# Kernel optimization log

Measured on AMD Instinct MI355X. Metric: run time of the kernel, lower is better.

## Reference

```python
import jax, jax.numpy as jnp
import numpy as np

HID = 4096
NH = 64
HD = HID // NH            # 64
ROT = int(0.5 * HD)       # 32, partial rotary
THETA = 25000.0
EPS = 1e-5
NEG = jnp.finfo(jnp.float32).min


def setup_inputs() -> dict:
    key = jax.random.key(0)
    ks = jax.random.split(key, 8)
    B, S = 1, 2048
    hidden_states = jax.random.normal(ks[0], (B, S, HID), dtype=jnp.float32)
    # causal additive mask [B,1,S,S]
    causal = jnp.where(jnp.tril(jnp.ones((S, S), dtype=bool)), 0.0, NEG)
    attention_mask = jnp.broadcast_to(causal, (B, 1, S, S)).astype(jnp.float32)
    position_ids = jnp.broadcast_to(jnp.arange(S, dtype=jnp.int32), (B, S))
    sc = 1.0 / np.sqrt(HID)
    W_qkv = jax.random.normal(ks[1], (HID, 3 * HID), dtype=jnp.float32) * sc
    b_qkv = jnp.zeros((3 * HID,), dtype=jnp.float32)
    W_dense = jax.random.normal(ks[2], (HID, HID), dtype=jnp.float32) * sc
    b_dense = jnp.zeros((HID,), dtype=jnp.float32)
    q_ln_w = jnp.ones((HD,), dtype=jnp.float32)
    q_ln_b = jnp.zeros((HD,), dtype=jnp.float32)
    k_ln_w = jnp.ones((HD,), dtype=jnp.float32)
    k_ln_b = jnp.zeros((HD,), dtype=jnp.float32)
    return dict(hidden_states=hidden_states, attention_mask=attention_mask,
                position_ids=position_ids, W_qkv=W_qkv, b_qkv=b_qkv,
                W_dense=W_dense, b_dense=b_dense,
                q_ln_w=q_ln_w, q_ln_b=q_ln_b, k_ln_w=k_ln_w, k_ln_b=k_ln_b)


def _layernorm(x, w, b):
    mu = jnp.mean(x, axis=-1, keepdims=True)
    var = jnp.mean(jnp.square(x - mu), axis=-1, keepdims=True)
    return (x - mu) * jax.lax.rsqrt(var + EPS) * w + b


def _rope_cos_sin(seq_len, position_ids):
    inv_freq = 1.0 / (THETA ** (jnp.arange(0, ROT, 2, dtype=jnp.float32) / ROT))
    t = jnp.arange(seq_len, dtype=jnp.float32)
    freqs = jnp.einsum('s,f->sf', t, inv_freq)        # [S, ROT/2]
    emb = jnp.concatenate([freqs, freqs], axis=-1)    # [S, ROT]
    cos = jnp.cos(emb)[position_ids][:, None, :, :]   # [B,1,S,ROT]
    sin = jnp.sin(emb)[position_ids][:, None, :, :]
    return cos, sin


def _rotate_half(x):
    x1, x2 = jnp.split(x, 2, axis=-1)
    return jnp.concatenate([-x2, x1], axis=-1)


def reference(hidden_states, attention_mask, position_ids, W_qkv, b_qkv,
              W_dense, b_dense, q_ln_w, q_ln_b, k_ln_w, k_ln_b):
    B, S, _ = hidden_states.shape
    fused = hidden_states @ W_qkv + b_qkv                 # [B,S,3*HID]
    fused = fused.reshape(B, S, NH, 3, HD)
    q, k, v = fused[..., 0, :], fused[..., 1, :], fused[..., 2, :]  # [B,S,NH,HD]
    q = _layernorm(q, q_ln_w, q_ln_b)
    k = _layernorm(k, k_ln_w, k_ln_b)
    q = q.transpose(0, 2, 1, 3)                           # [B,NH,S,HD]
    k = k.transpose(0, 2, 1, 3)
    v = v.transpose(0, 2, 1, 3)
    cos, sin = _rope_cos_sin(S, position_ids)
    q_rot, q_pass = q[..., :ROT], q[..., ROT:]
    k_rot, k_pass = k[..., :ROT], k[..., ROT:]
    q_rot = q_rot * cos + _rotate_half(q_rot) * sin
    k_rot = k_rot * cos + _rotate_half(k_rot) * sin
    q = jnp.concatenate([q_rot, q_pass], axis=-1)
    k = jnp.concatenate([k_rot, k_pass], axis=-1)
    scores = jnp.einsum('bhqd,bhkd->bhqk', q, k) / np.sqrt(HD)
    scores = scores + attention_mask
    probs = jax.nn.softmax(scores.astype(jnp.float32), axis=-1).astype(q.dtype)
    attn = jnp.einsum('bhqk,bhkd->bhqd', probs, v)        # [B,NH,S,HD]
    attn = attn.transpose(0, 2, 1, 3).reshape(B, S, HID)
    return attn @ W_dense + b_dense
```

## Files before the change

kernel.cpp:

```cpp
#include <hip/hip_runtime.h>
#include <hip/hip_bf16.h>


typedef __attribute__((ext_vector_type(4))) unsigned int u32x4;
typedef __attribute__((ext_vector_type(8))) __bf16 bf16x8;
typedef __attribute__((ext_vector_type(4))) float f32x4;

__device__ __forceinline__ bf16x8 frag_ld(const __hip_bfloat16* p) {
  return __builtin_bit_cast(bf16x8, *(const u32x4*)p);
}

__device__ __forceinline__ void gll16(const __hip_bfloat16* g,
                                      __hip_bfloat16* l) {
  __builtin_amdgcn_global_load_lds(
      (const __attribute__((address_space(1))) unsigned int*)g,
      (__attribute__((address_space(3))) unsigned int*)l, 16, 0, 0);
}

__global__ __launch_bounds__(256) void cvt_kernel(
    const float* __restrict__ in, __hip_bfloat16* __restrict__ out, int n4) {
  int i = blockIdx.x * 256 + threadIdx.x;
  if (i < n4) {
    float4 v = ((const float4*)in)[i];
    union { __hip_bfloat16 h[4]; unsigned long long u; } pk;
    pk.h[0] = __float2bfloat16(v.x);
    pk.h[1] = __float2bfloat16(v.y);
    pk.h[2] = __float2bfloat16(v.z);
    pk.h[3] = __float2bfloat16(v.w);
    ((unsigned long long*)out)[i] = pk.u;
  }
}

__global__ __launch_bounds__(256) void transpose_kernel(
    const float* __restrict__ W, __hip_bfloat16* __restrict__ WT,
    int K, int ldW, int colStride, int colOff) {
  __shared__ __align__(16) __hip_bfloat16 tile[64 * 72];
  const int t = threadIdx.x;
  const int c0 = blockIdx.x * colStride + colOff;
  const int n0 = blockIdx.x * 64;
  const int k0 = blockIdx.y * 64;
  for (int c = t; c < 1024; c += 256) {
    int row = c >> 4, col4 = (c & 15) << 2;
    float4 v = *(const float4*)&W[(size_t)(k0 + row) * ldW + c0 + col4];
    union { __hip_bfloat16 h[4]; unsigned long long u; } pk;
    pk.h[0] = __float2bfloat16(v.x);
    pk.h[1] = __float2bfloat16(v.y);
    pk.h[2] = __float2bfloat16(v.z);
    pk.h[3] = __float2bfloat16(v.w);
    *(unsigned long long*)&tile[row * 72 + col4] = pk.u;
  }
  __syncthreads();
  for (int c = t; c < 512; c += 256) {
    int row = c >> 3, col8 = (c & 7) << 3;
    union { __hip_bfloat16 h[8]; u32x4 v; } pk;
#pragma unroll
    for (int j = 0; j < 8; ++j) pk.h[j] = tile[(col8 + j) * 72 + row];
    *(u32x4*)&WT[(size_t)(n0 + row) * K + k0 + col8] = pk.v;
  }
}

__global__ __launch_bounds__(512, 2) void gemm256_kernel(
    const __hip_bfloat16* __restrict__ A, const __hip_bfloat16* __restrict__ BT,
    const float* __restrict__ bias, float* __restrict__ Cf,
    __hip_bfloat16* __restrict__ Cb, const float* __restrict__ lnw,
    const float* __restrict__ lnb, const int* __restrict__ pos,
    int M, int N, int K, int mode) {
  __shared__ __align__(16) __hip_bfloat16 As[3][128 * 64];
  __shared__ __align__(16) __hip_bfloat16 Bs[3][256 * 64];
  const int t = threadIdx.x;
  const int wv = t >> 6, lane = t & 63;
  const int qd = lane >> 4, md = lane & 15;
  const int wr = wv >> 2, wc = wv & 3;
  const int bid = blockIdx.x;
  const int swz = (bid & 7) * 32 + (bid >> 3);
  const int m0 = (swz >> 4) * 128, n0 = (swz & 15) * 256;
  const int rA = t >> 3;
  const int cg = (t & 7) ^ (rA & 7);
  const __hip_bfloat16* pA0 = A + (size_t)(m0 + rA) * K + cg * 8;
  const __hip_bfloat16* pA1 = A + (size_t)(m0 + 64 + rA) * K + cg * 8;
  const __hip_bfloat16* pB0 = BT + (size_t)(n0 + rA) * K + cg * 8;
  const __hip_bfloat16* pB1 = BT + (size_t)(n0 + 64 + rA) * K + cg * 8;
  const __hip_bfloat16* pB2 = BT + (size_t)(n0 + 128 + rA) * K + cg * 8;
  const __hip_bfloat16* pB3 = BT + (size_t)(n0 + 192 + rA) * K + cg * 8;
  const int ldsW = wv * 8 * 64;
  const int aRow = (wr * 64 + md) * 64;
  const int bRow = (wc * 64 + md) * 64;
  const int sw0 = (qd ^ (md & 7)) << 3;
  const int sw1 = ((4 + qd) ^ (md & 7)) << 3;
  f32x4 acc[4][4] = {};

  gll16(pA0, &As[0][ldsW]);
  gll16(pA1, &As[0][64 * 64 + ldsW]);
  gll16(pB0, &Bs[0][ldsW]);
  gll16(pB1, &Bs[0][64 * 64 + ldsW]);
  gll16(pB2, &Bs[0][128 * 64 + ldsW]);
  gll16(pB3, &Bs[0][192 * 64 + ldsW]);
  gll16(pA0 + 64, &As[1][ldsW]);
  gll16(pA1 + 64, &As[1][64 * 64 + ldsW]);
  gll16(pB0 + 64, &Bs[1][ldsW]);
  gll16(pB1 + 64, &Bs[1][64 * 64 + ldsW]);
  gll16(pB2 + 64, &Bs[1][128 * 64 + ldsW]);
  gll16(pB3 + 64, &Bs[1][192 * 64 + ldsW]);
  asm volatile("s_waitcnt vmcnt(6)" ::: "memory");
  __builtin_amdgcn_s_barrier();

  int cur = 0, nb = 2;
  for (int kt = 0; kt < 64; ++kt) {
    const __hip_bfloat16* Ac = As[cur];
    const __hip_bfloat16* Bc = Bs[cur];
    const bool st = kt < 62;
    const int koff = (kt + 2) * 64;
    bf16x8 af[4], bf[4];
#pragma unroll
    for (int i = 0; i < 4; ++i) af[i] = frag_ld(&Ac[aRow + i * 1024 + sw0]);
#pragma unroll
    for (int i = 0; i < 4; ++i) bf[i] = frag_ld(&Bc[bRow + i * 1024 + sw0]);
    if (st) {
      gll16(pA0 + koff, &As[nb][ldsW]);
      gll16(pA1 + koff, &As[nb][64 * 64 + ldsW]);
      gll16(pB0 + koff, &Bs[nb][ldsW]);
    }
    __builtin_amdgcn_s_barrier();
    asm volatile("s_waitcnt lgkmcnt(0)" ::: "memory");
    __builtin_amdgcn_s_setprio(1);
#pragma unroll
    for (int mi = 0; mi < 4; ++mi)
#pragma unroll
      for (int ni = 0; ni < 4; ++ni)
        acc[mi][ni] = __builtin_amdgcn_mfma_f32_16x16x32_bf16(
            af[mi], bf[ni], acc[mi][ni], 0, 0, 0);
    __builtin_amdgcn_s_setprio(0);
    __builtin_amdgcn_s_barrier();
#pragma unroll
    for (int i = 0; i < 4; ++i) af[i] = frag_ld(&Ac[aRow + i * 1024 + sw1]);
#pragma unroll
    for (int i = 0; i < 4; ++i) bf[i] = frag_ld(&Bc[bRow + i * 1024 + sw1]);
    if (st) {
      gll16(pB1 + koff, &Bs[nb][64 * 64 + ldsW]);
      gll16(pB2 + koff, &Bs[nb][128 * 64 + ldsW]);
      gll16(pB3 + koff, &Bs[nb][192 * 64 + ldsW]);
    }
    __builtin_amdgcn_s_barrier();
    asm volatile("s_waitcnt lgkmcnt(0)" ::: "memory");
    __builtin_amdgcn_s_setprio(1);
#pragma unroll
    for (int mi = 0; mi < 4; ++mi)
#pragma unroll
      for (int ni = 0; ni < 4; ++ni)
        acc[mi][ni] = __builtin_amdgcn_mfma_f32_16x16x32_bf16(
            af[mi], bf[ni], acc[mi][ni], 0, 0, 0);
    __builtin_amdgcn_s_setprio(0);
    if (kt < 62)
      asm volatile("s_waitcnt vmcnt(6)" ::: "memory");
    else if (kt < 63)
      asm volatile("s_waitcnt vmcnt(0)" ::: "memory");
    __builtin_amdgcn_s_barrier();
    cur = (cur == 2) ? 0 : cur + 1;
    nb = (nb == 2) ? 0 : nb + 1;
  }
  if (mode == 0) {
#pragma unroll
    for (int ni = 0; ni < 4; ++ni) {
      int col = n0 + wc * 64 + ni * 16 + md;
      float bv = bias[col];
#pragma unroll
      for (int mi = 0; mi < 4; ++mi) {
        int rb = m0 + wr * 64 + mi * 16 + qd * 4;
#pragma unroll
        for (int r = 0; r < 4; ++r)
          Cf[(size_t)(rb + r) * N + col] = acc[mi][ni][r] + bv;
      }
    }
  } else {
    float g[4], bb[4], bv[4];
    int hd[4];
#pragma unroll
    for (int ni = 0; ni < 4; ++ni) {
      int col = n0 + wc * 64 + ni * 16 + md;
      hd[ni] = col;
      bv[ni] = bias[(col >> 6) * 192 + (col & 63)];
      if (mode >= 2) { g[ni] = lnw[ni * 16 + md]; bb[ni] = lnb[ni * 16 + md]; }
    }
    const float invf =
        (mode >= 2) ? powf(25000.0f, -(float)md / 16.0f) : 0.0f;
#pragma unroll
    for (int mi = 0; mi < 4; ++mi) {
#pragma unroll
      for (int r = 0; r < 4; ++r) {
        int row = m0 + wr * 64 + mi * 16 + qd * 4 + r;
        float v[4];
#pragma unroll
        for (int ni = 0; ni < 4; ++ni) v[ni] = acc[mi][ni][r] + bv[ni];
        if (mode >= 2) {
          float s = v[0] + v[1] + v[2] + v[3];
#pragma unroll
          for (int x = 1; x < 16; x <<= 1) s += __shfl_xor(s, x, 16);
          float mu = s * (1.0f / 64.0f);
          float ss = 0.0f;
#pragma unroll
          for (int ni = 0; ni < 4; ++ni) {
            v[ni] -= mu;
            ss += v[ni] * v[ni];
          }
#pragma unroll
          for (int x = 1; x < 16; x <<= 1) ss += __shfl_xor(ss, x, 16);
          float rs = rsqrtf(ss * (1.0f / 64.0f) + 1e-5f);
#pragma unroll
          for (int ni = 0; ni < 4; ++ni) v[ni] = v[ni] * rs * g[ni] + bb[ni];
          float sn, cs;
          sincosf((float)pos[row] * invf, &sn, &cs);
          float v0 = v[0], v1 = v[1];
          v[0] = v0 * cs - v1 * sn;
          v[1] = v1 * cs + v0 * sn;
          if (mode == 2) {
#pragma unroll
            for (int ni = 0; ni < 4; ++ni) v[ni] *= 0.18033688f;
          }
        }
#pragma unroll
        for (int ni = 0; ni < 4; ++ni)
          Cb[((size_t)(hd[ni] >> 6) * M + row) * 64 + (hd[ni] & 63)] =
              __float2bfloat16(v[ni]);
      }
    }
  }
}

__global__ __launch_bounds__(256) void vtrans_kernel(
    const __hip_bfloat16* __restrict__ V, __hip_bfloat16* __restrict__ VT) {
  const int h = blockIdx.x, s0 = blockIdx.y * 64, t = threadIdx.x;
  __shared__ __align__(16) __hip_bfloat16 vt[64 * 72];
  for (int c = t; c < 512; c += 256) {
    int r = c >> 3, col8 = (c & 7) << 3;
    *(u32x4*)&vt[r * 72 + col8] =
        *(const u32x4*)&V[((size_t)h * 2048 + s0 + r) * 64 + col8];
  }
  __syncthreads();
  for (int c = t; c < 512; c += 256) {
    int d = c >> 3, col8 = (c & 7) << 3;
    union { __hip_bfloat16 hh[8]; u32x4 v; } pk;
#pragma unroll
    for (int j = 0; j < 8; ++j) pk.hh[j] = vt[(col8 + j) * 72 + d];
    *(u32x4*)&VT[((size_t)h * 64 + d) * 2048 + s0 + col8] = pk.v;
  }
}

__global__ __launch_bounds__(256) void fattn_kernel(
    const __hip_bfloat16* __restrict__ Q, const __hip_bfloat16* __restrict__ K,
    const __hip_bfloat16* __restrict__ VT, __hip_bfloat16* __restrict__ attn) {
  const int h = blockIdx.x, qb = 31 - blockIdx.y;
  const int t = threadIdx.x, wv = t >> 6, lane = t & 63;
  const int qd = lane >> 4, md = lane & 15;
  __shared__ __align__(16) __hip_bfloat16 Kls[64 * 72];
  __shared__ __align__(16) __hip_bfloat16 Vls[64 * 72];
  __shared__ __align__(16) __hip_bfloat16 Pls[64 * 72];
  const int q0 = qb * 64;
  const __hip_bfloat16* Qp = Q + ((size_t)h * 2048 + q0 + wv * 16 + md) * 64;
  bf16x8 qf0 = frag_ld(Qp + qd * 8);
  bf16x8 qf1 = frag_ld(Qp + 32 + qd * 8);
  float lp[4] = {0.f, 0.f, 0.f, 0.f};
  f32x4 O[4] = {};
  for (int kb = 0; kb <= qb; ++kb) {
    __syncthreads();
    for (int c = t; c < 512; c += 256) {
      int row = c >> 3, col8 = (c & 7) << 3;
      *(u32x4*)&Kls[row * 72 + col8] =
          *(const u32x4*)&K[((size_t)h * 2048 + kb * 64 + row) * 64 + col8];
      *(u32x4*)&Vls[row * 72 + col8] =
          *(const u32x4*)&VT[((size_t)h * 64 + row) * 2048 + kb * 64 + col8];
    }
    __syncthreads();
    const bool diag = (kb == qb);
    float pv[4][4];
#pragma unroll
    for (int nt = 0; nt < 4; ++nt) {
      f32x4 s4 = {};
      bf16x8 kf0 = frag_ld(&Kls[(nt * 16 + md) * 72 + qd * 8]);
      bf16x8 kf1 = frag_ld(&Kls[(nt * 16 + md) * 72 + 32 + qd * 8]);
      s4 = __builtin_amdgcn_mfma_f32_16x16x32_bf16(qf0, kf0, s4, 0, 0, 0);
      s4 = __builtin_amdgcn_mfma_f32_16x16x32_bf16(qf1, kf1, s4, 0, 0, 0);
      int key = nt * 16 + md;
#pragma unroll
      for (int r = 0; r < 4; ++r) {
        float p = exp2f(s4[r]);
        if (diag) p = (key > wv * 16 + qd * 4 + r) ? 0.f : p;
        pv[nt][r] = p;
        lp[r] += p;
      }
    }
#pragma unroll
    for (int nt = 0; nt < 4; ++nt)
#pragma unroll
      for (int r = 0; r < 4; ++r)
        Pls[(wv * 16 + qd * 4 + r) * 72 + nt * 16 + md] =
            __float2bfloat16(pv[nt][r]);
    bf16x8 pf0 = frag_ld(&Pls[(wv * 16 + md) * 72 + qd * 8]);
    bf16x8 pf1 = frag_ld(&Pls[(wv * 16 + md) * 72 + 32 + qd * 8]);
#pragma unroll
    for (int nt = 0; nt < 4; ++nt) {
      bf16x8 vf0 = frag_ld(&Vls[(nt * 16 + md) * 72 + qd * 8]);
      bf16x8 vf1 = frag_ld(&Vls[(nt * 16 + md) * 72 + 32 + qd * 8]);
      O[nt] = __builtin_amdgcn_mfma_f32_16x16x32_bf16(pf0, vf0, O[nt], 0, 0, 0);
      O[nt] = __builtin_amdgcn_mfma_f32_16x16x32_bf16(pf1, vf1, O[nt], 0, 0, 0);
    }
  }
#pragma unroll
  for (int r = 0; r < 4; ++r) {
#pragma unroll
    for (int x = 1; x < 16; x <<= 1) lp[r] += __shfl_xor(lp[r], x, 16);
    lp[r] = 1.0f / lp[r];
  }
#pragma unroll
  for (int nt = 0; nt < 4; ++nt) {
    int col = h * 64 + nt * 16 + md;
#pragma unroll
    for (int r = 0; r < 4; ++r) {
      int row = q0 + wv * 16 + qd * 4 + r;
      attn[(size_t)row * 4096 + col] = __float2bfloat16(O[nt][r] * lp[r]);
    }
  }
}

extern "C" void kernel_launch(void* const* d_in, const int* in_sizes, int n_in,
                              void* d_out, int out_size, void* d_ws,
                              size_t ws_size, hipStream_t stream) {
  const float* hidden = (const float*)d_in[0];
  const int* pos = (const int*)d_in[2];
  const float* Wqkv = (const float*)d_in[3];
  const float* bqkv = (const float*)d_in[4];
  const float* Wd = (const float*)d_in[5];
  const float* bd = (const float*)d_in[6];
  const float* qlw = (const float*)d_in[7];
  const float* qlb = (const float*)d_in[8];
  const float* klw = (const float*)d_in[9];
  const float* klb = (const float*)d_in[10];

  char* ws = (char*)d_ws;
  __hip_bfloat16* WpT = (__hip_bfloat16*)ws;
  __hip_bfloat16* VT = (__hip_bfloat16*)ws;
  __hip_bfloat16* attn = (__hip_bfloat16*)(ws + 16777216);
  __hip_bfloat16* Hb = (__hip_bfloat16*)(ws + 33554432);
  __hip_bfloat16* Qb = (__hip_bfloat16*)(ws + 50331648);
  __hip_bfloat16* Kb = (__hip_bfloat16*)(ws + 67108864);
  __hip_bfloat16* Vb = (__hip_bfloat16*)(ws + 83886080);
  __hip_bfloat16* WdT = (__hip_bfloat16*)(ws + 33554432);
  float* out = (float*)d_out;

  cvt_kernel<<<8192, 256, 0, stream>>>(hidden, Hb, 2097152);
  __hip_bfloat16* qkv_dst[3] = {Qb, Kb, Vb};
  const float* lnw_p[3] = {qlw, klw, nullptr};
  const float* lnb_p[3] = {qlb, klb, nullptr};
  const int mode_p[3] = {2, 3, 1};
  for (int p = 0; p < 3; ++p) {
    transpose_kernel<<<dim3(64, 64), 256, 0, stream>>>(Wqkv, WpT, 4096, 12288,
                                                       192, p * 64);
    gemm256_kernel<<<256, 512, 0, stream>>>(Hb, WpT, bqkv + p * 64, nullptr,
                                            qkv_dst[p], lnw_p[p], lnb_p[p], pos,
                                            2048, 4096, 4096, mode_p[p]);
  }
  vtrans_kernel<<<dim3(64, 32), 256, 0, stream>>>(Vb, VT);
  fattn_kernel<<<dim3(64, 32), 256, 0, stream>>>(Qb, Kb, VT, attn);
  transpose_kernel<<<dim3(64, 64), 256, 0, stream>>>(Wd, WdT, 4096, 4096, 64, 0);
  gemm256_kernel<<<256, 512, 0, stream>>>(attn, WdT, bd, out, nullptr, nullptr,
                                          nullptr, nullptr, 2048, 4096, 4096,
                                          0);
}
```

Baseline: 762.6 us.

## Use 16-wave 1024-thread GEMM blocks with smaller per-wave tiles

Reworks the GEMM kernel to launch 1024 threads per block instead of 512. The 128x256 block tile stays the same, but each wave now computes 32x64 instead of 64x64, so it holds half the accumulators and issues fewer global-to-LDS loads per stage. The aim is more waves per CU for latency hiding within the same LDS triple buffer. In exchange, each wave does less MFMA work per LDS fragment load and per barrier, so barrier and LDS-read overhead rise relative to compute.

```diff
diff --git a/kernel.cpp b/kernel.cpp
--- a/kernel.cpp
+++ b/kernel.cpp
@@ -59,7 +59,7 @@
   }
 }
 
-__global__ __launch_bounds__(512, 2) void gemm256_kernel(
+__global__ __launch_bounds__(1024, 1) void gemm256_kernel(
     const __hip_bfloat16* __restrict__ A, const __hip_bfloat16* __restrict__ BT,
     const float* __restrict__ bias, float* __restrict__ Cf,
     __hip_bfloat16* __restrict__ Cb, const float* __restrict__ lnw,
@@ -72,36 +72,29 @@
   const int qd = lane >> 4, md = lane & 15;
   const int wr = wv >> 2, wc = wv & 3;
   const int bid = blockIdx.x;
-  const int swz = (bid & 7) * 32 + (bid >> 3);
-  const int m0 = (swz >> 4) * 128, n0 = (swz & 15) * 256;
+  const int cpx = gridDim.x >> 3;
+  const int swz = (bid & 7) * cpx + (bid >> 3);
+  const int nblk = N >> 8;
+  const int m0 = (swz / nblk) * 128, n0 = (swz % nblk) * 256;
   const int rA = t >> 3;
   const int cg = (t & 7) ^ (rA & 7);
-  const __hip_bfloat16* pA0 = A + (size_t)(m0 + rA) * K + cg * 8;
-  const __hip_bfloat16* pA1 = A + (size_t)(m0 + 64 + rA) * K + cg * 8;
+  const __hip_bfloat16* pA = A + (size_t)(m0 + rA) * K + cg * 8;
   const __hip_bfloat16* pB0 = BT + (size_t)(n0 + rA) * K + cg * 8;
-  const __hip_bfloat16* pB1 = BT + (size_t)(n0 + 64 + rA) * K + cg * 8;
-  const __hip_bfloat16* pB2 = BT + (size_t)(n0 + 128 + rA) * K + cg * 8;
-  const __hip_bfloat16* pB3 = BT + (size_t)(n0 + 192 + rA) * K + cg * 8;
-  const int ldsW = wv * 8 * 64;
-  const int aRow = (wr * 64 + md) * 64;
+  const __hip_bfloat16* pB1 = pB0 + (size_t)128 * K;
+  const int ldsW = wv * 512;
+  const int aRow = (wr * 32 + md) * 64;
   const int bRow = (wc * 64 + md) * 64;
   const int sw0 = (qd ^ (md & 7)) << 3;
   const int sw1 = ((4 + qd) ^ (md & 7)) << 3;
-  f32x4 acc[4][4] = {};
-
-  gll16(pA0, &As[0][ldsW]);
-  gll16(pA1, &As[0][64 * 64 + ldsW]);
+  f32x4 acc[2][4] = {};
+
+  gll16(pA, &As[0][ldsW]);
   gll16(pB0, &Bs[0][ldsW]);
-  gll16(pB1, &Bs[0][64 * 64 + ldsW]);
-  gll16(pB2, &Bs[0][128 * 64 + ldsW]);
-  gll16(pB3, &Bs[0][192 * 64 + ldsW]);
-  gll16(pA0 + 64, &As[1][ldsW]);
-  gll16(pA1 + 64, &As[1][64 * 64 + ldsW]);
+  gll16(pB1, &Bs[0][8192 + ldsW]);
+  gll16(pA + 64, &As[1][ldsW]);
   gll16(pB0 + 64, &Bs[1][ldsW]);
-  gll16(pB1 + 64, &Bs[1][64 * 64 + ldsW]);
-  gll16(pB2 + 64, &Bs[1][128 * 64 + ldsW]);
-  gll16(pB3 + 64, &Bs[1][192 * 64 + ldsW]);
-  asm volatile("s_waitcnt vmcnt(6)" ::: "memory");
+  gll16(pB1 + 64, &Bs[1][8192 + ldsW]);
+  asm volatile("s_waitcnt vmcnt(3)" ::: "memory");
   __builtin_amdgcn_s_barrier();
 
   int cur = 0, nb = 2;
@@ -110,21 +103,20 @@
     const __hip_bfloat16* Bc = Bs[cur];
     const bool st = kt < 62;
     const int koff = (kt + 2) * 64;
-    bf16x8 af[4], bf[4];
-#pragma unroll
-    for (int i = 0; i < 4; ++i) af[i] = frag_ld(&Ac[aRow + i * 1024 + sw0]);
+    bf16x8 af[2], bf[4];
+#pragma unroll
+    for (int i = 0; i < 2; ++i) af[i] = frag_ld(&Ac[aRow + i * 1024 + sw0]);
 #pragma unroll
     for (int i = 0; i < 4; ++i) bf[i] = frag_ld(&Bc[bRow + i * 1024 + sw0]);
     if (st) {
-      gll16(pA0 + koff, &As[nb][ldsW]);
-      gll16(pA1 + koff, &As[nb][64 * 64 + ldsW]);
+      gll16(pA + koff, &As[nb][ldsW]);
       gll16(pB0 + koff, &Bs[nb][ldsW]);
     }
     __builtin_amdgcn_s_barrier();
     asm volatile("s_waitcnt lgkmcnt(0)" ::: "memory");
     __builtin_amdgcn_s_setprio(1);
 #pragma unroll
-    for (int mi = 0; mi < 4; ++mi)
+    for (int mi = 0; mi < 2; ++mi)
 #pragma unroll
       for (int ni = 0; ni < 4; ++ni)
         acc[mi][ni] = __builtin_amdgcn_mfma_f32_16x16x32_bf16(
@@ -132,26 +124,24 @@
     __builtin_amdgcn_s_setprio(0);
     __builtin_amdgcn_s_barrier();
 #pragma unroll
-    for (int i = 0; i < 4; ++i) af[i] = frag_ld(&Ac[aRow + i * 1024 + sw1]);
+    for (int i = 0; i < 2; ++i) af[i] = frag_ld(&Ac[aRow + i * 1024 + sw1]);
 #pragma unroll
     for (int i = 0; i < 4; ++i) bf[i] = frag_ld(&Bc[bRow + i * 1024 + sw1]);
     if (st) {
-      gll16(pB1 + koff, &Bs[nb][64 * 64 + ldsW]);
-      gll16(pB2 + koff, &Bs[nb][128 * 64 + ldsW]);
-      gll16(pB3 + koff, &Bs[nb][192 * 64 + ldsW]);
+      gll16(pB1 + koff, &Bs[nb][8192 + ldsW]);
     }
     __builtin_amdgcn_s_barrier();
     asm volatile("s_waitcnt lgkmcnt(0)" ::: "memory");
     __builtin_amdgcn_s_setprio(1);
 #pragma unroll
-    for (int mi = 0; mi < 4; ++mi)
+    for (int mi = 0; mi < 2; ++mi)
 #pragma unroll
       for (int ni = 0; ni < 4; ++ni)
         acc[mi][ni] = __builtin_amdgcn_mfma_f32_16x16x32_bf16(
             af[mi], bf[ni], acc[mi][ni], 0, 0, 0);
     __builtin_amdgcn_s_setprio(0);
     if (kt < 62)
-      asm volatile("s_waitcnt vmcnt(6)" ::: "memory");
+      asm volatile("s_waitcnt vmcnt(3)" ::: "memory");
     else if (kt < 63)
       asm volatile("s_waitcnt vmcnt(0)" ::: "memory");
     __builtin_amdgcn_s_barrier();
@@ -164,8 +154,8 @@
       int col = n0 + wc * 64 + ni * 16 + md;
       float bv = bias[col];
 #pragma unroll
-      for (int mi = 0; mi < 4; ++mi) {
-        int rb = m0 + wr * 64 + mi * 16 + qd * 4;
+      for (int mi = 0; mi < 2; ++mi) {
+        int rb = m0 + wr * 32 + mi * 16 + qd * 4;
 #pragma unroll
         for (int r = 0; r < 4; ++r)
           Cf[(size_t)(rb + r) * N + col] = acc[mi][ni][r] + bv;
@@ -184,10 +174,10 @@
     const float invf =
         (mode >= 2) ? powf(25000.0f, -(float)md / 16.0f) : 0.0f;
 #pragma unroll
-    for (int mi = 0; mi < 4; ++mi) {
+    for (int mi = 0; mi < 2; ++mi) {
 #pragma unroll
       for (int r = 0; r < 4; ++r) {
-        int row = m0 + wr * 64 + mi * 16 + qd * 4 + r;
+        int row = m0 + wr * 32 + mi * 16 + qd * 4 + r;
         float v[4];
 #pragma unroll
         for (int ni = 0; ni < 4; ++ni) v[ni] = acc[mi][ni][r] + bv[ni];
@@ -354,14 +344,14 @@
   for (int p = 0; p < 3; ++p) {
     transpose_kernel<<<dim3(64, 64), 256, 0, stream>>>(Wqkv, WpT, 4096, 12288,
                                                        192, p * 64);
-    gemm256_kernel<<<256, 512, 0, stream>>>(Hb, WpT, bqkv + p * 64, nullptr,
-                                            qkv_dst[p], lnw_p[p], lnb_p[p], pos,
-                                            2048, 4096, 4096, mode_p[p]);
+    gemm256_kernel<<<256, 1024, 0, stream>>>(Hb, WpT, bqkv + p * 64, nullptr,
+                                             qkv_dst[p], lnw_p[p], lnb_p[p],
+                                             pos, 2048, 4096, 4096, mode_p[p]);
   }
   vtrans_kernel<<<dim3(64, 32), 256, 0, stream>>>(Vb, VT);
   fattn_kernel<<<dim3(64, 32), 256, 0, stream>>>(Qb, Kb, VT, attn);
   transpose_kernel<<<dim3(64, 64), 256, 0, stream>>>(Wd, WdT, 4096, 4096, 64, 0);
-  gemm256_kernel<<<256, 512, 0, stream>>>(attn, WdT, bd, out, nullptr, nullptr,
-                                          nullptr, nullptr, 2048, 4096, 4096,
-                                          0);
-}
+  gemm256_kernel<<<256, 1024, 0, stream>>>(attn, WdT, bd, out, nullptr, nullptr,
+                                           nullptr, nullptr, 2048, 4096, 4096,
+                                           0);
+}
```

Result: no change. 771.4 us (+1.2%).

## Double query tile per attention block to share K/V tile loads across 8 waves

Applied to the files above, without the earlier changes.

The flash-attention kernel now covers 128 query rows per block with 512 threads (two 64-row groups of four waves) and launches half as many blocks. Each K/V tile staged in LDS is reused by twice as many queries, which roughly halves global K/V traffic and shared-memory staging per query. Each wave gets its own P scratch buffer. The upper query group idles on the last key tile but still hits the barriers, and larger blocks mean fewer blocks in flight and a coarser causal load balance.

```diff
diff --git a/kernel.cpp b/kernel.cpp
--- a/kernel.cpp
+++ b/kernel.cpp
@@ -245,32 +245,35 @@
   }
 }
 
-__global__ __launch_bounds__(256) void fattn_kernel(
+__global__ __launch_bounds__(512) void fattn_kernel(
     const __hip_bfloat16* __restrict__ Q, const __hip_bfloat16* __restrict__ K,
     const __hip_bfloat16* __restrict__ VT, __hip_bfloat16* __restrict__ attn) {
-  const int h = blockIdx.x, qb = 31 - blockIdx.y;
+  const int h = blockIdx.x, qb = 15 - blockIdx.y;
   const int t = threadIdx.x, wv = t >> 6, lane = t & 63;
+  const int g = wv >> 2, w4 = wv & 3;
   const int qd = lane >> 4, md = lane & 15;
   __shared__ __align__(16) __hip_bfloat16 Kls[64 * 72];
   __shared__ __align__(16) __hip_bfloat16 Vls[64 * 72];
-  __shared__ __align__(16) __hip_bfloat16 Pls[64 * 72];
-  const int q0 = qb * 64;
-  const __hip_bfloat16* Qp = Q + ((size_t)h * 2048 + q0 + wv * 16 + md) * 64;
+  __shared__ __align__(16) __hip_bfloat16 Pls[8][16 * 72];
+  const int q0 = qb * 128;
+  const __hip_bfloat16* Qp =
+      Q + ((size_t)h * 2048 + q0 + g * 64 + w4 * 16 + md) * 64;
   bf16x8 qf0 = frag_ld(Qp + qd * 8);
   bf16x8 qf1 = frag_ld(Qp + 32 + qd * 8);
   float lp[4] = {0.f, 0.f, 0.f, 0.f};
   f32x4 O[4] = {};
-  for (int kb = 0; kb <= qb; ++kb) {
+  const int srow = t >> 3, scol = (t & 7) << 3;
+  const int kdiag = 2 * qb + g;
+  const int kbmax = 2 * qb + 1;
+  for (int kb = 0; kb <= kbmax; ++kb) {
     __syncthreads();
-    for (int c = t; c < 512; c += 256) {
-      int row = c >> 3, col8 = (c & 7) << 3;
-      *(u32x4*)&Kls[row * 72 + col8] =
-          *(const u32x4*)&K[((size_t)h * 2048 + kb * 64 + row) * 64 + col8];
-      *(u32x4*)&Vls[row * 72 + col8] =
-          *(const u32x4*)&VT[((size_t)h * 64 + row) * 2048 + kb * 64 + col8];
-    }
+    *(u32x4*)&Kls[srow * 72 + scol] =
+        *(const u32x4*)&K[((size_t)h * 2048 + kb * 64 + srow) * 64 + scol];
+    *(u32x4*)&Vls[srow * 72 + scol] =
+        *(const u32x4*)&VT[((size_t)h * 64 + srow) * 2048 + kb * 64 + scol];
     __syncthreads();
-    const bool diag = (kb == qb);
+    if (kb > kdiag) continue;
+    const bool diag = (kb == kdiag);
     float pv[4][4];
 #pragma unroll
     for (int nt = 0; nt < 4; ++nt) {
@@ -283,7 +286,7 @@
 #pragma unroll
       for (int r = 0; r < 4; ++r) {
         float p = exp2f(s4[r]);
-        if (diag) p = (key > wv * 16 + qd * 4 + r) ? 0.f : p;
+        if (diag) p = (key > w4 * 16 + qd * 4 + r) ? 0.f : p;
         pv[nt][r] = p;
         lp[r] += p;
       }
@@ -292,10 +295,10 @@
     for (int nt = 0; nt < 4; ++nt)
 #pragma unroll
       for (int r = 0; r < 4; ++r)
-        Pls[(wv * 16 + qd * 4 + r) * 72 + nt * 16 + md] =
+        Pls[wv][(qd * 4 + r) * 72 + nt * 16 + md] =
             __float2bfloat16(pv[nt][r]);
-    bf16x8 pf0 = frag_ld(&Pls[(wv * 16 + md) * 72 + qd * 8]);
-    bf16x8 pf1 = frag_ld(&Pls[(wv * 16 + md) * 72 + 32 + qd * 8]);
+    bf16x8 pf0 = frag_ld(&Pls[wv][md * 72 + qd * 8]);
+    bf16x8 pf1 = frag_ld(&Pls[wv][md * 72 + 32 + qd * 8]);
 #pragma unroll
     for (int nt = 0; nt < 4; ++nt) {
       bf16x8 vf0 = frag_ld(&Vls[(nt * 16 + md) * 72 + qd * 8]);
@@ -315,7 +318,7 @@
     int col = h * 64 + nt * 16 + md;
 #pragma unroll
     for (int r = 0; r < 4; ++r) {
-      int row = q0 + wv * 16 + qd * 4 + r;
+      int row = q0 + g * 64 + w4 * 16 + qd * 4 + r;
       attn[(size_t)row * 4096 + col] = __float2bfloat16(O[nt][r] * lp[r]);
     }
   }
@@ -359,7 +362,7 @@
                                             2048, 4096, 4096, mode_p[p]);
   }
   vtrans_kernel<<<dim3(64, 32), 256, 0, stream>>>(Vb, VT);
-  fattn_kernel<<<dim3(64, 32), 256, 0, stream>>>(Qb, Kb, VT, attn);
+  fattn_kernel<<<dim3(64, 16), 512, 0, stream>>>(Qb, Kb, VT, attn);
   transpose_kernel<<<dim3(64, 64), 256, 0, stream>>>(Wd, WdT, 4096, 4096, 64, 0);
   gemm256_kernel<<<256, 512, 0, stream>>>(attn, WdT, bd, out, nullptr, nullptr,
                                           nullptr, nullptr, 2048, 4096, 4096,
```

After: 770.8 us. Within noise of the previous version (+1.1%).
